# Kernel tuning notes

Hardware: AMD Instinct MI355X
Metric: run time of the kernel (lower is better)

Reference implementation:

```python
import jax, jax.numpy as jnp
import numpy as np

L = 2        # lstm layers (encoder == decoder, required since h0/c0 are shared)
H = 512      # neural_size
FEAT = 128   # encoder input feature size
T_ENC = 512  # encoder sequence length
B = 512      # batch
PRED_LEN = 96


def _lstm_cell(x, h, c, W_ih, W_hh, b_ih, b_hh):
    # PyTorch gate order: i, f, g, o
    gates = x @ W_ih.T + b_ih + h @ W_hh.T + b_hh
    i, f, g, o = jnp.split(gates, 4, axis=-1)
    i = jax.nn.sigmoid(i)
    f = jax.nn.sigmoid(f)
    g = jnp.tanh(g)
    o = jax.nn.sigmoid(o)
    c_new = f * c + i * g
    h_new = o * jnp.tanh(c_new)
    return h_new, c_new


def _multilayer_step(layer_params, x, h, c):
    # h, c: [L, B, H]; x: [B, in]; loop over fixed small layer count
    hs, cs = [], []
    inp = x
    for l, (W_ih, W_hh, b_ih, b_hh) in enumerate(layer_params):
        h_new, c_new = _lstm_cell(inp, h[l], c[l], W_ih, W_hh, b_ih, b_hh)
        hs.append(h_new)
        cs.append(c_new)
        inp = h_new
    return inp, jnp.stack(hs), jnp.stack(cs)


def setup_inputs() -> dict:
    key = jax.random.key(0)
    ks = jax.random.split(key, 24)
    s = 0.1  # weight init scale
    inp = {
        "X_encode": jax.random.normal(ks[0], (B, T_ENC, FEAT), jnp.float32),
        "X_decode": jax.random.normal(ks[1], (B, PRED_LEN, 8), jnp.float32),
        "y": jax.random.normal(ks[2], (B, PRED_LEN, 1), jnp.float32),
        "tf_mask": jax.random.randint(ks[3], (PRED_LEN,), 0, 2, jnp.int32),
    }
    # encoder LSTM params (layer 0 in=FEAT, layer 1 in=H)
    inp["enc_W_ih0"] = jax.random.normal(ks[4], (4 * H, FEAT), jnp.float32) * s
    inp["enc_W_hh0"] = jax.random.normal(ks[5], (4 * H, H), jnp.float32) * s
    inp["enc_b_ih0"] = jax.random.normal(ks[6], (4 * H,), jnp.float32) * s
    inp["enc_b_hh0"] = jax.random.normal(ks[7], (4 * H,), jnp.float32) * s
    inp["enc_W_ih1"] = jax.random.normal(ks[8], (4 * H, H), jnp.float32) * s
    inp["enc_W_hh1"] = jax.random.normal(ks[9], (4 * H, H), jnp.float32) * s
    inp["enc_b_ih1"] = jax.random.normal(ks[10], (4 * H,), jnp.float32) * s
    inp["enc_b_hh1"] = jax.random.normal(ks[11], (4 * H,), jnp.float32) * s
    # decoder LSTM params (layer 0 in=1, layer 1 in=H)
    inp["dec_W_ih0"] = jax.random.normal(ks[12], (4 * H, 1), jnp.float32) * s
    inp["dec_W_hh0"] = jax.random.normal(ks[13], (4 * H, H), jnp.float32) * s
    inp["dec_b_ih0"] = jax.random.normal(ks[14], (4 * H,), jnp.float32) * s
    inp["dec_b_hh0"] = jax.random.normal(ks[15], (4 * H,), jnp.float32) * s
    inp["dec_W_ih1"] = jax.random.normal(ks[16], (4 * H, H), jnp.float32) * s
    inp["dec_W_hh1"] = jax.random.normal(ks[17], (4 * H, H), jnp.float32) * s
    inp["dec_b_ih1"] = jax.random.normal(ks[18], (4 * H,), jnp.float32) * s
    inp["dec_b_hh1"] = jax.random.normal(ks[19], (4 * H,), jnp.float32) * s
    # output projection
    inp["fc_W"] = jax.random.normal(ks[20], (1, H), jnp.float32) * s
    inp["fc_b"] = jax.random.normal(ks[21], (1,), jnp.float32) * s
    return inp


def reference(X_encode, X_decode, y, tf_mask,
              enc_W_ih0, enc_W_hh0, enc_b_ih0, enc_b_hh0,
              enc_W_ih1, enc_W_hh1, enc_b_ih1, enc_b_hh1,
              dec_W_ih0, dec_W_hh0, dec_b_ih0, dec_b_hh0,
              dec_W_ih1, dec_W_hh1, dec_b_ih1, dec_b_hh1,
              fc_W, fc_b):
    enc_params = [(enc_W_ih0, enc_W_hh0, enc_b_ih0, enc_b_hh0),
                  (enc_W_ih1, enc_W_hh1, enc_b_ih1, enc_b_hh1)]
    dec_params = [(dec_W_ih0, dec_W_hh0, dec_b_ih0, dec_b_hh0),
                  (dec_W_ih1, dec_W_hh1, dec_b_ih1, dec_b_hh1)]

    batch = X_encode.shape[0]
    h0 = jnp.zeros((L, batch, H), X_encode.dtype)
    c0 = jnp.zeros((L, batch, H), X_encode.dtype)

    # ---- encoder: scan over time, keep only final (h, c) ----
    def enc_step(carry, x_t):
        h, c = carry
        _, h, c = _multilayer_step(enc_params, x_t, h, c)
        return (h, c), None

    (h, c), _ = jax.lax.scan(enc_step, (h0, c0), jnp.swapaxes(X_encode, 0, 1))

    # ---- decoder initial input: sum(sum(X_decode, 1), 1).unsqueeze(-1) ----
    dec_in0 = jnp.sum(X_decode, axis=(1, 2))[:, None]  # (B, 1)

    # teacher forcing: y[:, t+1, :] when tf and t < pred_len-1, else own output
    y_next = jnp.concatenate([y[:, 1:, :], jnp.zeros_like(y[:, :1, :])], axis=1)
    tf = (tf_mask != 0) & (jnp.arange(PRED_LEN) < PRED_LEN - 1)

    def dec_step(carry, xs):
        inp, h, c = carry
        tf_t, y_t = xs  # scalar bool, (B, 1)
        top, h, c = _multilayer_step(dec_params, inp, h, c)
        out = top @ fc_W.T + fc_b  # (B, 1)
        nxt = jnp.where(tf_t, y_t, out)
        return (nxt, h, c), out

    _, outs = jax.lax.scan(dec_step, (dec_in0, h, c),
                           (tf, jnp.swapaxes(y_next, 0, 1)))
    final_out = jnp.swapaxes(outs, 0, 1)  # (B, pred_len, 1)
    return final_out
```

## Files before the change

kernel.cpp:

```cpp
#include <hip/hip_runtime.h>


typedef unsigned int u32;
typedef unsigned short u16;

using bf16x8  = __attribute__((ext_vector_type(8))) __bf16;
using u16x8   = __attribute__((ext_vector_type(8))) u16;
using floatx4 = __attribute__((ext_vector_type(4))) float;

#define NWG 256
#define HB  262144

#define ENC0_PLANE ((size_t)2048 * 640)
#define ENC1_PLANE ((size_t)2048 * 1024)
#define DEC0_PLANE ((size_t)2048 * 512)
#define DEC1_PLANE ((size_t)2048 * 1024)

#define H0_CHUNK 0
#define H1_CHUNK 4096
#define LO_BYTES 32768

#define AS1C(p) ((const __attribute__((address_space(1))) void*)(p))
#define AS3(p)  ((__attribute__((address_space(3))) void*)(u32)(size_t)(p))

__device__ __forceinline__ u16 f2bf(float f) {
  u32 u = __builtin_bit_cast(u32, f);
  u += 0x7FFFu + ((u >> 16) & 1u);
  return (u16)(u >> 16);
}
__device__ __forceinline__ float bf2f(u16 h) {
  return __builtin_bit_cast(float, (u32)h << 16);
}
__device__ __forceinline__ bf16x8 ld8(const u16* p) {
  return __builtin_bit_cast(bf16x8, *reinterpret_cast<const u16x8*>(p));
}
__device__ __forceinline__ float sig_(float x) {
  x = fminf(fmaxf(x, -30.f), 30.f);
  return 1.f / (1.f + __expf(-x));
}
__device__ __forceinline__ float tanh_(float x) {
  x = fminf(fmaxf(x, -15.f), 15.f);
  float e = __expf(2.f * x);
  return (e - 1.f) / (e + 1.f);
}

#define MFMA(a, b, c) __builtin_amdgcn_mfma_f32_16x16x32_bf16((a), (b), (c), 0, 0, 0)

__device__ __forceinline__ void gemm_lds(floatx4* acc, const char* apb,
    const u16* __restrict__ Wseg, size_t wplane, int strideW,
    int j0, int l15, int quad, int kbeg, int kend)
{
  const u16* wp = Wseg + (size_t)(j0 + l15) * strideW + (quad << 3);
  const size_t gs = (size_t)strideW << 9;
  #pragma unroll 2
  for (int k = kbeg; k < kend; k += 32) {
    const int kb8 = ((k >> 3) + quad) << 9;
    bf16x8 ah = *reinterpret_cast<const bf16x8*>(apb + kb8);
    bf16x8 al = *reinterpret_cast<const bf16x8*>(apb + kb8 + LO_BYTES);
    #pragma unroll
    for (int g = 0; g < 4; ++g) {
      bf16x8 wh = ld8(wp + k + g * gs);
      bf16x8 wl = ld8(wp + k + g * gs + wplane);
      acc[g] = MFMA(ah, wh, acc[g]);
      acc[g] = MFMA(ah, wl, acc[g]);
      acc[g] = MFMA(al, wh, acc[g]);
    }
  }
}

__device__ __forceinline__ void gemm_x128s(floatx4* acc,
    const float* __restrict__ X, int t,
    const u16* __restrict__ Wseg, size_t wplane, int strideW,
    int row0, int j0, int lane)
{
  const int quad = lane >> 4, l15 = lane & 15;
  const float* xp = X + ((size_t)(row0 + l15) * 512 + t) * 128 + (quad << 3);
  const u16* wp = Wseg + (size_t)(j0 + l15) * strideW + (quad << 3);
  const size_t gs = (size_t)strideW << 9;
  #pragma unroll
  for (int k = 0; k < 128; k += 32) {
    floatx4 xa = *reinterpret_cast<const floatx4*>(xp + k);
    floatx4 xb_ = *reinterpret_cast<const floatx4*>(xp + k + 4);
    u16x8 uh, ul;
    #pragma unroll
    for (int i = 0; i < 4; ++i) {
      u16 h0 = f2bf(xa[i]);  uh[i] = h0;     ul[i] = f2bf(xa[i] - bf2f(h0));
      u16 h1 = f2bf(xb_[i]); uh[4 + i] = h1; ul[4 + i] = f2bf(xb_[i] - bf2f(h1));
    }
    bf16x8 ah = __builtin_bit_cast(bf16x8, uh);
    bf16x8 al = __builtin_bit_cast(bf16x8, ul);
    #pragma unroll
    for (int g = 0; g < 4; ++g) {
      bf16x8 wh = ld8(wp + k + g * gs);
      bf16x8 wl = ld8(wp + k + g * gs + wplane);
      acc[g] = MFMA(ah, wh, acc[g]);
      acc[g] = MFMA(ah, wl, acc[g]);
      acc[g] = MFMA(al, wh, acc[g]);
    }
  }
}

__device__ __forceinline__ void store_h_split(u16* __restrict__ hout,
                                              size_t off, float h) {
  u16 hh = f2bf(h);
  u16 hl = f2bf(h - bf2f(hh));
  __hip_atomic_store(hout + off,      hh, __ATOMIC_RELAXED, __HIP_MEMORY_SCOPE_AGENT);
  __hip_atomic_store(hout + off + HB, hl, __ATOMIC_RELAXED, __HIP_MEMORY_SCOPE_AGENT);
}

__device__ __forceinline__ void cell_store(const floatx4* acc,
    float* __restrict__ c, u16* __restrict__ hout,
    const float* __restrict__ bs, int row0, int j0, int lane)
{
  const int quad = lane >> 4, l15 = lane & 15;
  const int col = j0 + l15;
  const float bi = bs[col], bff = bs[512 + col], bg = bs[1024 + col], bo = bs[1536 + col];
  const int r0 = row0 + (quad << 2);
  #pragma unroll
  for (int r = 0; r < 4; ++r) {
    const size_t off = ((size_t)(r0 + r) << 9) + col;
    float ii = sig_(acc[0][r] + bi);
    float ff = sig_(acc[1][r] + bff);
    float gg = tanh_(acc[2][r] + bg);
    float oo = sig_(acc[3][r] + bo);
    float cn = ff * c[off] + ii * gg;
    c[off] = cn;
    store_h_split(hout, off, oo * tanh_(cn));
  }
}

__device__ __forceinline__ void cell_store_dec0(const floatx4* acc,
    float* __restrict__ c, u16* __restrict__ hout,
    const float* __restrict__ bs, const float* __restrict__ w0col,
    const float* __restrict__ din0, const float* __restrict__ y,
    const int* __restrict__ tfm, float* __restrict__ dout,
    int t, int row0, int j0, int lane)
{
  const int quad = lane >> 4, l15 = lane & 15;
  const int col = j0 + l15;
  const float bi = bs[col], bff = bs[512 + col], bg = bs[1024 + col], bo = bs[1536 + col];
  const float wi = w0col[col], wf = w0col[512 + col], wg = w0col[1024 + col], wo = w0col[1536 + col];
  const int r0 = row0 + (quad << 2);
  #pragma unroll
  for (int r = 0; r < 4; ++r) {
    const int row = r0 + r;
    float inp;
    if (t == 0) inp = din0[row];
    else if (tfm[t - 1] != 0) inp = y[row * 96 + t];
    else inp = __hip_atomic_load(dout + row * 96 + (t - 1),
                                 __ATOMIC_RELAXED, __HIP_MEMORY_SCOPE_AGENT);
    const size_t off = ((size_t)row << 9) + col;
    float ii = sig_(acc[0][r] + bi + inp * wi);
    float ff = sig_(acc[1][r] + bff + inp * wf);
    float gg = tanh_(acc[2][r] + bg + inp * wg);
    float oo = sig_(acc[3][r] + bo + inp * wo);
    float cn = ff * c[off] + ii * gg;
    c[off] = cn;
    store_h_split(hout, off, oo * tanh_(cn));
  }
}

__device__ __forceinline__ void cell_store_dec1(const floatx4* acc,
    float* __restrict__ c, u16* __restrict__ hout,
    const float* __restrict__ bs, const float* __restrict__ fcW,
    const float* __restrict__ fcb, float* __restrict__ dout,
    int t, int row0, int j0, int lane)
{
  const int quad = lane >> 4, l15 = lane & 15;
  const int col = j0 + l15;
  const float bi = bs[col], bff = bs[512 + col], bg = bs[1024 + col], bo = bs[1536 + col];
  const float fw = fcW[col];
  const int r0 = row0 + (quad << 2);
  float s[4];
  #pragma unroll
  for (int r = 0; r < 4; ++r) {
    const size_t off = ((size_t)(r0 + r) << 9) + col;
    float ii = sig_(acc[0][r] + bi);
    float ff = sig_(acc[1][r] + bff);
    float gg = tanh_(acc[2][r] + bg);
    float oo = sig_(acc[3][r] + bo);
    float cn = ff * c[off] + ii * gg;
    c[off] = cn;
    float h = oo * tanh_(cn);
    store_h_split(hout, off, h);
    s[r] = h * fw;
  }
  #pragma unroll
  for (int m = 1; m < 16; m <<= 1) {
    #pragma unroll
    for (int r = 0; r < 4; ++r) s[r] += __shfl_xor(s[r], m, 64);
  }
  if (l15 == 0) {
    #pragma unroll
    for (int r = 0; r < 4; ++r) {
      float v = s[r];
      if (j0 == 0) v += fcb[0];
      atomicAdd(&dout[(size_t)(r0 + r) * 96 + t], v);
    }
  }
}

__global__ __launch_bounds__(512) void seq2seq_persist(
    const float* __restrict__ Xenc, const float* __restrict__ y,
    const int* __restrict__ tfm, const float* __restrict__ dWih0col,
    const float* __restrict__ fcW, const float* __restrict__ fcb,
    const u16* __restrict__ enc0, const u16* __restrict__ enc1,
    const u16* __restrict__ dec0w, const u16* __restrict__ dec1,
    u16* __restrict__ h0bufs, u16* __restrict__ h1bufs,
    float* __restrict__ c0, float* __restrict__ c1,
    const float* __restrict__ bsum, const float* __restrict__ din0,
    float* __restrict__ dout, u32* __restrict__ bar)
{
  extern __shared__ char smem_c[];
  const int tid = threadIdx.x;
  const int g = blockIdx.x;
  const int wave = tid >> 6, lane = tid & 63;
  const int w4 = wave & 3, kh = wave >> 2;
  const int quad = lane >> 4, l15 = lane & 15;
  const int q = g >> 3;
  const int hj_tile = (g & 7) + ((q & 1) << 3);
  const int b_tile = q >> 1;
  const int b0 = b_tile << 5, hj0 = hj_tile << 5;
  const int row0 = b0 + ((w4 & 1) << 4);
  const int j0 = hj0 + ((w4 >> 1) << 4);
  const int slot = g & 7;
  u16* h0buf[2] = { h0bufs, h0bufs + 2 * HB };
  u16* h1buf[2] = { h1bufs, h1bufs + 2 * HB };
  unsigned ep = 0;

  const int lrow = ((w4 & 1) << 4) + l15;
  const char* apb0 = smem_c + lrow * 16;
  const char* apb1 = smem_c + 65536 + lrow * 16;
  floatx4* xb = (floatx4*)smem_c;
  #define XR(w4_, L_, g_) (((((w4_) * 2 + (L_)) * 4 + (g_)) << 6) + lane)

  auto stage = [&](const u16* hbuf, int region_chunk) {
    #pragma unroll
    for (int blk = 0; blk < 8; ++blk) {
      const int cw = (blk << 9) + (wave << 6);
      const int c  = cw + lane;
      const int half = c >> 11, cc = c & 2047;
      const int k8 = cc >> 5, row = cc & 31;
      const u16* src = hbuf + (size_t)half * HB
                     + ((size_t)(b0 + row) << 9) + (k8 << 3);
      __builtin_amdgcn_global_load_lds(
          AS1C(src), AS3(smem_c + (size_t)(region_chunk + cw) * 16),
          16, 0, 0x11 );
    }
  };

  auto gbar = [&]() {
    __syncthreads();
    ++ep;
    if (tid == 0) {
      u32 prev = __hip_atomic_fetch_add(&bar[slot * 32], 1u,
                     __ATOMIC_RELAXED, __HIP_MEMORY_SCOPE_AGENT);
      if (prev == ep * 32u - 1u) {
        u32 pm = __hip_atomic_fetch_add(&bar[256], 1u,
                     __ATOMIC_RELAXED, __HIP_MEMORY_SCOPE_AGENT);
        if (pm == ep * 8u - 1u)
          __hip_atomic_store(&bar[288], ep,
                     __ATOMIC_RELAXED, __HIP_MEMORY_SCOPE_AGENT);
      }
      while (__hip_atomic_load(&bar[288],
                 __ATOMIC_RELAXED, __HIP_MEMORY_SCOPE_AGENT) < ep)
        __builtin_amdgcn_s_sleep(1);
    }
    asm volatile("" ::: "memory");
    __syncthreads();
  };

  for (int p = 0; p <= 512; ++p) {
    const int cur = p & 1, nxt = cur ^ 1;
    stage(h0buf[cur], H0_CHUNK);
    stage(h1buf[cur], H1_CHUNK);
    __syncthreads();
    floatx4 a1[4] = { floatx4{0,0,0,0}, floatx4{0,0,0,0}, floatx4{0,0,0,0}, floatx4{0,0,0,0} };
    floatx4 a0[4] = { floatx4{0,0,0,0}, floatx4{0,0,0,0}, floatx4{0,0,0,0}, floatx4{0,0,0,0} };
    if (p >= 1) {
      if (kh == 0) {
        gemm_lds(a1, apb0, enc1,       ENC1_PLANE, 1024, j0, l15, quad, 0, 256);
        gemm_lds(a1, apb1, enc1 + 512, ENC1_PLANE, 1024, j0, l15, quad, 0, 256);
      } else {
        gemm_lds(a1, apb0, enc1,       ENC1_PLANE, 1024, j0, l15, quad, 256, 512);
        gemm_lds(a1, apb1, enc1 + 512, ENC1_PLANE, 1024, j0, l15, quad, 256, 512);
      }
    }
    if (p <= 511) {
      if (kh == 0) {
        gemm_x128s(a0, Xenc, p, enc0, ENC0_PLANE, 640, row0, j0, lane);
        gemm_lds(a0, apb0, enc0 + 128, ENC0_PLANE, 640, j0, l15, quad, 0, 192);
      } else {
        gemm_lds(a0, apb0, enc0 + 128, ENC0_PLANE, 640, j0, l15, quad, 192, 512);
      }
    }
    __syncthreads();
    if (kh == 1) {
      for (int gg = 0; gg < 4; ++gg) xb[XR(w4, 0, gg)] = a1[gg];
      for (int gg = 0; gg < 4; ++gg) xb[XR(w4, 1, gg)] = a0[gg];
    }
    __syncthreads();
    if (kh == 0) {
      if (p >= 1) {
        for (int gg = 0; gg < 4; ++gg) a1[gg] += xb[XR(w4, 0, gg)];
        cell_store(a1, c1, h1buf[nxt], bsum + 2048, row0, j0, lane);
      }
      if (p <= 511) {
        for (int gg = 0; gg < 4; ++gg) a0[gg] += xb[XR(w4, 1, gg)];
        cell_store(a0, c0, h0buf[nxt], bsum, row0, j0, lane);
      }
    }
    gbar();
  }

  int cur0 = 0, cur1 = 1;
  for (int t = 0; t < 96; ++t) {
    {
      stage(h0buf[cur0], H0_CHUNK);
      __syncthreads();
      floatx4 acc[4] = { floatx4{0,0,0,0}, floatx4{0,0,0,0}, floatx4{0,0,0,0}, floatx4{0,0,0,0} };
      if (kh == 0) gemm_lds(acc, apb0, dec0w, DEC0_PLANE, 512, j0, l15, quad, 0, 256);
      else         gemm_lds(acc, apb0, dec0w, DEC0_PLANE, 512, j0, l15, quad, 256, 512);
      __syncthreads();
      if (kh == 1) {
        for (int gg = 0; gg < 4; ++gg) xb[XR(w4, 0, gg)] = acc[gg];
      }
      __syncthreads();
      if (kh == 0) {
        for (int gg = 0; gg < 4; ++gg) acc[gg] += xb[XR(w4, 0, gg)];
        cell_store_dec0(acc, c0, h0buf[cur0 ^ 1], bsum + 4096, dWih0col,
                        din0, y, tfm, dout, t, row0, j0, lane);
      }
    }
    gbar();
    cur0 ^= 1;
    {
      stage(h0buf[cur0], H0_CHUNK);
      stage(h1buf[cur1], H1_CHUNK);
      __syncthreads();
      floatx4 acc[4] = { floatx4{0,0,0,0}, floatx4{0,0,0,0}, floatx4{0,0,0,0}, floatx4{0,0,0,0} };
      if (kh == 0) {
        gemm_lds(acc, apb0, dec1,       DEC1_PLANE, 1024, j0, l15, quad, 0, 256);
        gemm_lds(acc, apb1, dec1 + 512, DEC1_PLANE, 1024, j0, l15, quad, 0, 256);
      } else {
        gemm_lds(acc, apb0, dec1,       DEC1_PLANE, 1024, j0, l15, quad, 256, 512);
        gemm_lds(acc, apb1, dec1 + 512, DEC1_PLANE, 1024, j0, l15, quad, 256, 512);
      }
      __syncthreads();
      if (kh == 1) {
        for (int gg = 0; gg < 4; ++gg) xb[XR(w4, 0, gg)] = acc[gg];
      }
      __syncthreads();
      if (kh == 0) {
        for (int gg = 0; gg < 4; ++gg) acc[gg] += xb[XR(w4, 0, gg)];
        cell_store_dec1(acc, c1, h1buf[cur1 ^ 1], bsum + 6144, fcW, fcb,
                        dout, t, row0, j0, lane);
      }
    }
    gbar();
    cur1 ^= 1;
  }
}

__global__ void prep_misc(float* c0, float* c1, u16* h0b, u16* h1b,
    float* dout, u32* bar, float* bsum,
    const float* ebih0, const float* ebhh0, const float* ebih1, const float* ebhh1,
    const float* dbih0, const float* dbhh0, const float* dbih1, const float* dbhh1,
    const float* Xdec, float* din0)
{
  const int idx = blockIdx.x * 256 + threadIdx.x;
  c0[idx] = 0.f; c1[idx] = 0.f;
  h0b[idx] = 0; h0b[idx + HB] = 0; h0b[idx + 2 * HB] = 0; h0b[idx + 3 * HB] = 0;
  h1b[idx] = 0; h1b[idx + HB] = 0; h1b[idx + 2 * HB] = 0; h1b[idx + 3 * HB] = 0;
  if (idx < 49152) dout[idx] = 0.f;
  if (idx < 8192) {
    const int which = idx >> 11, j = idx & 2047;
    float v;
    if (which == 0)      v = ebih0[j] + ebhh0[j];
    else if (which == 1) v = ebih1[j] + ebhh1[j];
    else if (which == 2) v = dbih0[j] + dbhh0[j];
    else                 v = dbih1[j] + dbhh1[j];
    bsum[idx] = v;
  }
  if (idx < 512) {
    float s = 0.f;
    const float* p = Xdec + (size_t)idx * 768;
    for (int i = 0; i < 768; ++i) s += p[i];
    din0[idx] = s;
  }
  if (idx < 512) bar[idx] = 0u;
}

__device__ __forceinline__ void wsplit(u16* dst, size_t plane, size_t i, float w) {
  u16 hh = f2bf(w);
  dst[i] = hh;
  dst[i + plane] = f2bf(w - bf2f(hh));
}

__global__ void prep_weights(u16* enc0, const float* eWih0, const float* eWhh0,
    u16* enc1, const float* eWih1, const float* eWhh1,
    u16* dec0, const float* dWhh0,
    u16* dec1, const float* dWih1, const float* dWhh1)
{
  const int idx = blockIdx.x * 256 + threadIdx.x;
  if (idx < 2048 * 640) {
    const int j = idx / 640, k = idx - j * 640;
    wsplit(enc0, ENC0_PLANE, idx,
           k < 128 ? eWih0[j * 128 + k] : eWhh0[j * 512 + (k - 128)]);
  }
  {
    const int j = idx >> 10, k = idx & 1023;
    wsplit(enc1, ENC1_PLANE, idx,
           k < 512 ? eWih1[(j << 9) + k] : eWhh1[(j << 9) + k - 512]);
    wsplit(dec1, DEC1_PLANE, idx,
           k < 512 ? dWih1[(j << 9) + k] : dWhh1[(j << 9) + k - 512]);
  }
  if (idx < 2048 * 512) wsplit(dec0, DEC0_PLANE, idx, dWhh0[idx]);
}

extern "C" void kernel_launch(void* const* d_in, const int* in_sizes, int n_in,
                              void* d_out, int out_size, void* d_ws, size_t ws_size,
                              hipStream_t stream)
{
  const float* Xenc  = (const float*)d_in[0];
  const float* Xdec  = (const float*)d_in[1];
  const float* y     = (const float*)d_in[2];
  const int*   tfm   = (const int*)d_in[3];
  const float* eWih0 = (const float*)d_in[4];
  const float* eWhh0 = (const float*)d_in[5];
  const float* ebih0 = (const float*)d_in[6];
  const float* ebhh0 = (const float*)d_in[7];
  const float* eWih1 = (const float*)d_in[8];
  const float* eWhh1 = (const float*)d_in[9];
  const float* ebih1 = (const float*)d_in[10];
  const float* ebhh1 = (const float*)d_in[11];
  const float* dWih0 = (const float*)d_in[12];
  const float* dWhh0 = (const float*)d_in[13];
  const float* dbih0 = (const float*)d_in[14];
  const float* dbhh0 = (const float*)d_in[15];
  const float* dWih1 = (const float*)d_in[16];
  const float* dWhh1 = (const float*)d_in[17];
  const float* dbih1 = (const float*)d_in[18];
  const float* dbhh1 = (const float*)d_in[19];
  const float* fcW   = (const float*)d_in[20];
  const float* fcb   = (const float*)d_in[21];
  float* dout = (float*)d_out;

  char* base = (char*)d_ws;
  size_t off = 0;
  auto alloc = [&](size_t n) -> char* {
    char* p = base + off;
    off = (off + n + 255) & ~(size_t)255;
    return p;
  };
  u32* bar  = (u32*)alloc(512 * 4);
  u16* enc0 = (u16*)alloc(ENC0_PLANE * 2 * 2);
  u16* enc1 = (u16*)alloc(ENC1_PLANE * 2 * 2);
  u16* dec0 = (u16*)alloc(DEC0_PLANE * 2 * 2);
  u16* dec1 = (u16*)alloc(DEC1_PLANE * 2 * 2);
  u16* h0b  = (u16*)alloc((size_t)4 * HB * 2);
  u16* h1b  = (u16*)alloc((size_t)4 * HB * 2);
  float* c0 = (float*)alloc((size_t)HB * 4);
  float* c1 = (float*)alloc((size_t)HB * 4);
  float* bs = (float*)alloc((size_t)8192 * 4);
  float* di = (float*)alloc((size_t)512 * 4);

  static int lds_attr_set = 0;
  if (!lds_attr_set) {
    (void)hipFuncSetAttribute((const void*)seq2seq_persist,
        hipFuncAttributeMaxDynamicSharedMemorySize, 131072);
    lds_attr_set = 1;
  }

  prep_misc<<<1024, 256, 0, stream>>>(c0, c1, h0b, h1b, dout, bar, bs,
      ebih0, ebhh0, ebih1, ebhh1, dbih0, dbhh0, dbih1, dbhh1, Xdec, di);
  prep_weights<<<8192, 256, 0, stream>>>(enc0, eWih0, eWhh0, enc1, eWih1, eWhh1,
      dec0, dWhh0, dec1, dWih1, dWhh1);
  seq2seq_persist<<<NWG, 512, 131072, stream>>>(Xenc, y, tfm, dWih0, fcW, fcb,
      enc0, enc1, dec0, dec1, h0b, h1b, c0, c1, bs, di, dout, bar);
}
```

Baseline: 35.51 ms.

## Repack split-bf16 weights into per-hidden-tile contiguous regions with interleaved hi/lo rows

```diff
diff --git a/kernel.cpp b/kernel.cpp
--- a/kernel.cpp
+++ b/kernel.cpp
@@ -11,10 +11,10 @@
 #define NWG 256
 #define HB  262144
 
-#define ENC0_PLANE ((size_t)2048 * 640)
-#define ENC1_PLANE ((size_t)2048 * 1024)
-#define DEC0_PLANE ((size_t)2048 * 512)
-#define DEC1_PLANE ((size_t)2048 * 1024)
+#define ENC0_REG (128 * 2 * 640)
+#define ENC1_REG (128 * 2 * 1024)
+#define DEC0_REG (128 * 2 * 512)
+#define DEC1_REG (128 * 2 * 1024)
 
 #define H0_CHUNK 0
 #define H1_CHUNK 4096
@@ -47,11 +47,11 @@
 #define MFMA(a, b, c) __builtin_amdgcn_mfma_f32_16x16x32_bf16((a), (b), (c), 0, 0, 0)
 
 __device__ __forceinline__ void gemm_lds(floatx4* acc, const char* apb,
-    const u16* __restrict__ Wseg, size_t wplane, int strideW,
-    int j0, int l15, int quad, int kbeg, int kend)
-{
-  const u16* wp = Wseg + (size_t)(j0 + l15) * strideW + (quad << 3);
-  const size_t gs = (size_t)strideW << 9;
+    const u16* __restrict__ Wreg, int strideW,
+    int lj0, int l15, int quad, int kbeg, int kend)
+{
+  const u16* wp = Wreg + (size_t)(lj0 + l15) * 2 * strideW + (quad << 3);
+  const size_t gs = (size_t)strideW << 6;
   #pragma unroll 2
   for (int k = kbeg; k < kend; k += 32) {
     const int kb8 = ((k >> 3) + quad) << 9;
@@ -60,7 +60,7 @@
     #pragma unroll
     for (int g = 0; g < 4; ++g) {
       bf16x8 wh = ld8(wp + k + g * gs);
-      bf16x8 wl = ld8(wp + k + g * gs + wplane);
+      bf16x8 wl = ld8(wp + k + g * gs + strideW);
       acc[g] = MFMA(ah, wh, acc[g]);
       acc[g] = MFMA(ah, wl, acc[g]);
       acc[g] = MFMA(al, wh, acc[g]);
@@ -70,13 +70,13 @@
 
 __device__ __forceinline__ void gemm_x128s(floatx4* acc,
     const float* __restrict__ X, int t,
-    const u16* __restrict__ Wseg, size_t wplane, int strideW,
-    int row0, int j0, int lane)
+    const u16* __restrict__ Wreg, int strideW,
+    int row0, int lj0, int lane)
 {
   const int quad = lane >> 4, l15 = lane & 15;
   const float* xp = X + ((size_t)(row0 + l15) * 512 + t) * 128 + (quad << 3);
-  const u16* wp = Wseg + (size_t)(j0 + l15) * strideW + (quad << 3);
-  const size_t gs = (size_t)strideW << 9;
+  const u16* wp = Wreg + (size_t)(lj0 + l15) * 2 * strideW + (quad << 3);
+  const size_t gs = (size_t)strideW << 6;
   #pragma unroll
   for (int k = 0; k < 128; k += 32) {
     floatx4 xa = *reinterpret_cast<const floatx4*>(xp + k);
@@ -92,7 +92,7 @@
     #pragma unroll
     for (int g = 0; g < 4; ++g) {
       bf16x8 wh = ld8(wp + k + g * gs);
-      bf16x8 wl = ld8(wp + k + g * gs + wplane);
+      bf16x8 wl = ld8(wp + k + g * gs + strideW);
       acc[g] = MFMA(ah, wh, acc[g]);
       acc[g] = MFMA(ah, wl, acc[g]);
       acc[g] = MFMA(al, wh, acc[g]);
@@ -223,10 +223,16 @@
   const int b0 = b_tile << 5, hj0 = hj_tile << 5;
   const int row0 = b0 + ((w4 & 1) << 4);
   const int j0 = hj0 + ((w4 >> 1) << 4);
+  const int lj0 = (w4 >> 1) << 4;
   const int slot = g & 7;
   u16* h0buf[2] = { h0bufs, h0bufs + 2 * HB };
   u16* h1buf[2] = { h1bufs, h1bufs + 2 * HB };
   unsigned ep = 0;
+
+  const u16* enc0r = enc0  + (size_t)hj_tile * ENC0_REG;
+  const u16* enc1r = enc1  + (size_t)hj_tile * ENC1_REG;
+  const u16* dec0r = dec0w + (size_t)hj_tile * DEC0_REG;
+  const u16* dec1r = dec1  + (size_t)hj_tile * DEC1_REG;
 
   const int lrow = ((w4 & 1) << 4) + l15;
   const char* apb0 = smem_c + lrow * 16;
@@ -245,7 +251,7 @@
                      + ((size_t)(b0 + row) << 9) + (k8 << 3);
       __builtin_amdgcn_global_load_lds(
           AS1C(src), AS3(smem_c + (size_t)(region_chunk + cw) * 16),
-          16, 0, 0x11 );
+          16, 0, 0x13 );
     }
   };
 
@@ -279,19 +285,19 @@
     floatx4 a0[4] = { floatx4{0,0,0,0}, floatx4{0,0,0,0}, floatx4{0,0,0,0}, floatx4{0,0,0,0} };
     if (p >= 1) {
       if (kh == 0) {
-        gemm_lds(a1, apb0, enc1,       ENC1_PLANE, 1024, j0, l15, quad, 0, 256);
-        gemm_lds(a1, apb1, enc1 + 512, ENC1_PLANE, 1024, j0, l15, quad, 0, 256);
+        gemm_lds(a1, apb0, enc1r,       1024, lj0, l15, quad, 0, 256);
+        gemm_lds(a1, apb1, enc1r + 512, 1024, lj0, l15, quad, 0, 256);
       } else {
-        gemm_lds(a1, apb0, enc1,       ENC1_PLANE, 1024, j0, l15, quad, 256, 512);
-        gemm_lds(a1, apb1, enc1 + 512, ENC1_PLANE, 1024, j0, l15, quad, 256, 512);
+        gemm_lds(a1, apb0, enc1r,       1024, lj0, l15, quad, 256, 512);
+        gemm_lds(a1, apb1, enc1r + 512, 1024, lj0, l15, quad, 256, 512);
       }
     }
     if (p <= 511) {
       if (kh == 0) {
-        gemm_x128s(a0, Xenc, p, enc0, ENC0_PLANE, 640, row0, j0, lane);
-        gemm_lds(a0, apb0, enc0 + 128, ENC0_PLANE, 640, j0, l15, quad, 0, 192);
+        gemm_x128s(a0, Xenc, p, enc0r, 640, row0, lj0, lane);
+        gemm_lds(a0, apb0, enc0r + 128, 640, lj0, l15, quad, 0, 192);
       } else {
-        gemm_lds(a0, apb0, enc0 + 128, ENC0_PLANE, 640, j0, l15, quad, 192, 512);
+        gemm_lds(a0, apb0, enc0r + 128, 640, lj0, l15, quad, 192, 512);
       }
     }
     __syncthreads();
@@ -319,8 +325,8 @@
       stage(h0buf[cur0], H0_CHUNK);
       __syncthreads();
       floatx4 acc[4] = { floatx4{0,0,0,0}, floatx4{0,0,0,0}, floatx4{0,0,0,0}, floatx4{0,0,0,0} };
-      if (kh == 0) gemm_lds(acc, apb0, dec0w, DEC0_PLANE, 512, j0, l15, quad, 0, 256);
-      else         gemm_lds(acc, apb0, dec0w, DEC0_PLANE, 512, j0, l15, quad, 256, 512);
+      if (kh == 0) gemm_lds(acc, apb0, dec0r, 512, lj0, l15, quad, 0, 256);
+      else         gemm_lds(acc, apb0, dec0r, 512, lj0, l15, quad, 256, 512);
       __syncthreads();
       if (kh == 1) {
         for (int gg = 0; gg < 4; ++gg) xb[XR(w4, 0, gg)] = acc[gg];
@@ -340,11 +346,11 @@
       __syncthreads();
       floatx4 acc[4] = { floatx4{0,0,0,0}, floatx4{0,0,0,0}, floatx4{0,0,0,0}, floatx4{0,0,0,0} };
       if (kh == 0) {
-        gemm_lds(acc, apb0, dec1,       DEC1_PLANE, 1024, j0, l15, quad, 0, 256);
-        gemm_lds(acc, apb1, dec1 + 512, DEC1_PLANE, 1024, j0, l15, quad, 0, 256);
+        gemm_lds(acc, apb0, dec1r,       1024, lj0, l15, quad, 0, 256);
+        gemm_lds(acc, apb1, dec1r + 512, 1024, lj0, l15, quad, 0, 256);
       } else {
-        gemm_lds(acc, apb0, dec1,       DEC1_PLANE, 1024, j0, l15, quad, 256, 512);
-        gemm_lds(acc, apb1, dec1 + 512, DEC1_PLANE, 1024, j0, l15, quad, 256, 512);
+        gemm_lds(acc, apb0, dec1r,       1024, lj0, l15, quad, 256, 512);
+        gemm_lds(acc, apb1, dec1r + 512, 1024, lj0, l15, quad, 256, 512);
       }
       __syncthreads();
       if (kh == 1) {
@@ -391,10 +397,13 @@
   if (idx < 512) bar[idx] = 0u;
 }
 
-__device__ __forceinline__ void wsplit(u16* dst, size_t plane, size_t i, float w) {
+__device__ __forceinline__ void wsplit2(u16* dst, int S, int j_src, int k, float w) {
+  const int j = j_src & 511, gg = j_src >> 9;
+  const int hj = j >> 5, lj = j & 31;
+  const size_t base = (size_t)((hj << 7) + (gg << 5) + lj) * 2 * S + k;
   u16 hh = f2bf(w);
-  dst[i] = hh;
-  dst[i + plane] = f2bf(w - bf2f(hh));
+  dst[base] = hh;
+  dst[base + S] = f2bf(w - bf2f(hh));
 }
 
 __global__ void prep_weights(u16* enc0, const float* eWih0, const float* eWhh0,
@@ -405,17 +414,20 @@
   const int idx = blockIdx.x * 256 + threadIdx.x;
   if (idx < 2048 * 640) {
     const int j = idx / 640, k = idx - j * 640;
-    wsplit(enc0, ENC0_PLANE, idx,
-           k < 128 ? eWih0[j * 128 + k] : eWhh0[j * 512 + (k - 128)]);
+    wsplit2(enc0, 640, j, k,
+            k < 128 ? eWih0[j * 128 + k] : eWhh0[j * 512 + (k - 128)]);
   }
   {
     const int j = idx >> 10, k = idx & 1023;
-    wsplit(enc1, ENC1_PLANE, idx,
-           k < 512 ? eWih1[(j << 9) + k] : eWhh1[(j << 9) + k - 512]);
-    wsplit(dec1, DEC1_PLANE, idx,
-           k < 512 ? dWih1[(j << 9) + k] : dWhh1[(j << 9) + k - 512]);
-  }
-  if (idx < 2048 * 512) wsplit(dec0, DEC0_PLANE, idx, dWhh0[idx]);
+    wsplit2(enc1, 1024, j, k,
+            k < 512 ? eWih1[(j << 9) + k] : eWhh1[(j << 9) + k - 512]);
+    wsplit2(dec1, 1024, j, k,
+            k < 512 ? dWih1[(j << 9) + k] : dWhh1[(j << 9) + k - 512]);
+  }
+  if (idx < 2048 * 512) {
+    const int j = idx >> 9, k = idx & 511;
+    wsplit2(dec0, 512, j, k, dWhh0[idx]);
+  }
 }
 
 extern "C" void kernel_launch(void* const* d_in, const int* in_sizes, int n_in,
@@ -454,10 +466,10 @@
     return p;
   };
   u32* bar  = (u32*)alloc(512 * 4);
-  u16* enc0 = (u16*)alloc(ENC0_PLANE * 2 * 2);
-  u16* enc1 = (u16*)alloc(ENC1_PLANE * 2 * 2);
-  u16* dec0 = (u16*)alloc(DEC0_PLANE * 2 * 2);
-  u16* dec1 = (u16*)alloc(DEC1_PLANE * 2 * 2);
+  u16* enc0 = (u16*)alloc((size_t)ENC0_REG * 16 * 2);
+  u16* enc1 = (u16*)alloc((size_t)ENC1_REG * 16 * 2);
+  u16* dec0 = (u16*)alloc((size_t)DEC0_REG * 16 * 2);
+  u16* dec1 = (u16*)alloc((size_t)DEC1_REG * 16 * 2);
   u16* h0b  = (u16*)alloc((size_t)4 * HB * 2);
   u16* h1b  = (u16*)alloc((size_t)4 * HB * 2);
   float* c0 = (float*)alloc((size_t)HB * 4);
```

Result: slower. 38.88 ms (+9.5%).
